# Kernel tuning notes

Measured on AMD Instinct MI355X. Metric: run time of the kernel, lower is better.

The kernel has to match this reference:

```python
import jax, jax.numpy as jnp
import numpy as np

SIG = [1, 1, 1, 1, -1]  # Cl(4,1)
NVEC = 5
GA = 1 << NVEC  # 32


def _build_gp_table():
    # Cayley table for the geometric product on blades indexed by bitmask.
    G = np.zeros((GA, GA, GA), np.float32)
    for a in range(GA):
        for b in range(GA):
            s = 0
            t = a >> 1
            while t:
                s += bin(t & b).count('1')
                t >>= 1
            sign = -1.0 if (s & 1) else 1.0
            common = a & b
            for i in range(NVEC):
                if (common >> i) & 1:
                    sign *= SIG[i]
            G[a, b, a ^ b] = sign
    return G

GP_TABLE = jnp.asarray(_build_gp_table())


def geometric_product(x, y):
    return jnp.einsum('...i,...j,ijk->...k', x, y, GP_TABLE)


def manifold_norm(x):
    # normalize each multivector onto the unit sphere in R^32
    return x / (jnp.linalg.norm(x, axis=-1, keepdims=True) + 1e-6)


def versor_linear(x, W, b):
    # channel mixing shared across multivector components: x [..., in, ga]
    return jnp.einsum('...ig,oi->...og', x, W) + b


def layer_norm2d(x, w, b):
    # LayerNorm over last two dims [D, ga] jointly
    mu = jnp.mean(x, axis=(-2, -1), keepdims=True)
    var = jnp.var(x, axis=(-2, -1), keepdims=True)
    return (x - mu) / jnp.sqrt(var + 1e-5) * w + b


def attention(x, Wq, bq, Wk, bk, Wv, bv, Wo, bo, n_heads):
    B, S, D, G = x.shape
    dh = D // n_heads
    q = versor_linear(x, Wq, bq).reshape(B, S, n_heads, dh, G)
    k = versor_linear(x, Wk, bk).reshape(B, S, n_heads, dh, G)
    v = versor_linear(x, Wv, bv).reshape(B, S, n_heads, dh, G)
    scale = 1.0 / np.sqrt(dh * G).astype(np.float32)
    scores = jnp.einsum('bshdg,bthdg->bhst', q, k) * scale
    probs = jax.nn.softmax(scores, axis=-1)
    o = jnp.einsum('bhst,bthdg->bshdg', probs, v).reshape(B, S, D, G)
    return versor_linear(o, Wo, bo)


N_HEADS = 8


def forward(x, Wq, bq, Wk, bk, Wv, bv, Wo, bo, ln1_w, ln1_b, ln2_w, ln2_b,
            gamma1, gamma2, W1, b1, W2, b2, Wr, br, Wc, bc):
    L = Wq.shape[0]
    for l in range(L):
        h = attention(layer_norm2d(x, ln1_w[l], ln1_b[l]),
                      Wq[l], bq[l], Wk[l], bk[l], Wv[l], bv[l], Wo[l], bo[l], N_HEADS)
        x = manifold_norm(x + gamma1[l] * h)
        m = versor_linear(layer_norm2d(x, ln2_w[l], ln2_b[l]), W1[l], b1[l])
        m = versor_linear(jnp.tanh(m), W2[l], b2[l])
        x = manifold_norm(x + gamma2[l] * m)
    # RecursiveRotorAccumulator: log(S)-step inclusive scan of rotors
    delta = versor_linear(x, Wr, br)
    rot = 0.5 * delta
    rot = rot.at[..., 0].add(1.0)
    rot = manifold_norm(rot)
    S = x.shape[1]
    step = 1
    while step < S:
        left = rot[:, :-step]
        right = rot[:, step:]
        comb = manifold_norm(geometric_product(right, left))
        rot = jnp.concatenate([rot[:, :step], comb], axis=1)
        step *= 2
    pooled = rot[:, -1]  # [B, D, ga]
    logits = pooled.reshape(pooled.shape[0], -1) @ Wc.T + bc
    return logits


def setup_inputs() -> dict:
    key = jax.random.key(0)
    B, S, D, G, L, NC = 8, 256, 64, GA, 4, 1000
    E = 4 * D  # expansion hidden
    ks = jax.random.split(key, 16)
    sd = 0.02
    inp = {
        'x': jax.random.normal(ks[0], (B, S, D, G), jnp.float32),
        'Wq': jax.random.normal(ks[1], (L, D, D), jnp.float32) * sd,
        'bq': jnp.zeros((L, D, G), jnp.float32),
        'Wk': jax.random.normal(ks[2], (L, D, D), jnp.float32) * sd,
        'bk': jnp.zeros((L, D, G), jnp.float32),
        'Wv': jax.random.normal(ks[3], (L, D, D), jnp.float32) * sd,
        'bv': jnp.zeros((L, D, G), jnp.float32),
        'Wo': jax.random.normal(ks[4], (L, D, D), jnp.float32) * sd,
        'bo': jnp.zeros((L, D, G), jnp.float32),
        'ln1_w': jnp.ones((L, D, G), jnp.float32),
        'ln1_b': jnp.zeros((L, D, G), jnp.float32),
        'ln2_w': jnp.ones((L, D, G), jnp.float32),
        'ln2_b': jnp.zeros((L, D, G), jnp.float32),
        'gamma1': 1e-5 * jnp.ones((L, D, G), jnp.float32),
        'gamma2': 1e-5 * jnp.ones((L, D, G), jnp.float32),
        'W1': jax.random.normal(ks[5], (L, E, D), jnp.float32) * sd,
        'b1': jnp.zeros((L, E, G), jnp.float32),
        'W2': jax.random.normal(ks[6], (L, D, E), jnp.float32) * sd,
        'b2': jnp.zeros((L, D, G), jnp.float32),
        'Wr': jax.random.normal(ks[7], (D, D), jnp.float32) * sd,
        'br': jnp.zeros((D, G), jnp.float32),
        'Wc': jax.random.normal(ks[8], (NC, D * G), jnp.float32) * sd,
        'bc': jnp.zeros((NC,), jnp.float32),
    }
    return inp


def reference(x, Wq, bq, Wk, bk, Wv, bv, Wo, bo, ln1_w, ln1_b, ln2_w, ln2_b,
              gamma1, gamma2, W1, b1, W2, b2, Wr, br, Wc, bc):
    return forward(x, Wq, bq, Wk, bk, Wv, bv, Wo, bo, ln1_w, ln1_b, ln2_w, ln2_b,
                   gamma1, gamma2, W1, b1, W2, b2, Wr, br, Wc, bc)
```

## Files before the change

kernel.cpp:

```cpp
#include <hip/hip_runtime.h>
#include <hip/hip_bf16.h>

constexpr int kB  = 8;
constexpr int kS  = 256;
constexpr int kD  = 64;
constexpr int kG  = 32;
constexpr int kE  = 256;
constexpr int kNH = 8;
constexpr int kHD = 256;
constexpr int kDG = kD * kG;
constexpr int kT  = kB * kS;
constexpr int kNC = 1000;

using bf16x8 = __attribute__((ext_vector_type(8))) short;
using f32x4  = __attribute__((ext_vector_type(4))) float;

__device__ __forceinline__ short f2bf(float f) {
    unsigned u = __float_as_uint(f);
    unsigned r = (u + 0x7FFFu + ((u >> 16) & 1u)) >> 16;
    return (short)r;
}

__device__ __forceinline__ float tanh_fast(float x) {
    float a = fabsf(x);
    float e = __expf(-2.f * a);
    float t = (1.f - e) / (1.f + e);
    return copysignf(t, x);
}

__global__ __launch_bounds__(256) void ln_kernel(const float* __restrict__ Xin,
                                                 const float* __restrict__ w,
                                                 const float* __restrict__ b,
                                                 float* __restrict__ A) {
    int t = blockIdx.x, tid = threadIdx.x;
    const float* xp = Xin + (size_t)t * kDG;
    __shared__ float r1[256], r2[256];
    float v[8], s = 0.f, ss = 0.f;
#pragma unroll
    for (int j = 0; j < 8; j++) {
        float x = xp[tid + j * 256];
        v[j] = x; s += x; ss += x * x;
    }
    r1[tid] = s; r2[tid] = ss; __syncthreads();
    for (int o = 128; o > 0; o >>= 1) {
        if (tid < o) { r1[tid] += r1[tid + o]; r2[tid] += r2[tid + o]; }
        __syncthreads();
    }
    float mean = r1[0] * (1.f / kDG);
    float var  = r2[0] * (1.f / kDG) - mean * mean;
    float rstd = rsqrtf(var + 1e-5f);
    float* ao = A + (size_t)t * kDG;
#pragma unroll
    for (int j = 0; j < 8; j++) {
        int jj = tid + j * 256;
        ao[jj] = (v[j] - mean) * rstd * w[jj] + b[jj];
    }
}

__device__ __forceinline__ void epi_res_mn_ln(
    const f32x4 (&acc)[4][2], const float* __restrict__ bias,
    const float* __restrict__ Xin, float* __restrict__ Xout,
    const float* __restrict__ gamma,
    const float* __restrict__ lnw, const float* __restrict__ lnb,
    float* __restrict__ Aout, int tok, int l16, int quad, bool do_ln) {
    const size_t tb = (size_t)tok * kDG;
    float xv[4][2][4];
    float s = 0.f, ss = 0.f;
#pragma unroll
    for (int mt = 0; mt < 4; ++mt)
#pragma unroll
        for (int r = 0; r < 4; ++r) {
            int o = mt * 16 + quad * 4 + r;
            float vv[2]; float sq = 0.f;
#pragma unroll
            for (int nt = 0; nt < 2; ++nt) {
                int g = nt * 16 + l16;
                float h = acc[mt][nt][r] + bias[o * kG + g];
                float v = Xin[tb + o * kG + g] + gamma[o * kG + g] * h;
                vv[nt] = v; sq = fmaf(v, v, sq);
            }
#pragma unroll
            for (int off = 1; off < 16; off <<= 1) sq += __shfl_xor(sq, off, 64);
            float rn = 1.f / (sqrtf(sq) + 1e-6f);
#pragma unroll
            for (int nt = 0; nt < 2; ++nt) {
                int g = nt * 16 + l16;
                float x = vv[nt] * rn;
                xv[mt][nt][r] = x;
                Xout[tb + o * kG + g] = x;
                s += x; ss = fmaf(x, x, ss);
            }
        }
    if (!do_ln) return;
#pragma unroll
    for (int off = 1; off < 64; off <<= 1) {
        s += __shfl_xor(s, off, 64); ss += __shfl_xor(ss, off, 64);
    }
    float mean = s * (1.f / kDG);
    float var  = ss * (1.f / kDG) - mean * mean;
    float rstd = rsqrtf(var + 1e-5f);
#pragma unroll
    for (int mt = 0; mt < 4; ++mt)
#pragma unroll
        for (int nt = 0; nt < 2; ++nt) {
            int g = nt * 16 + l16;
#pragma unroll
            for (int r = 0; r < 4; ++r) {
                int o = mt * 16 + quad * 4 + r;
                Aout[tb + o * kG + g] = (xv[mt][nt][r] - mean) * rstd * lnw[o * kG + g] + lnb[o * kG + g];
            }
        }
}

__global__ __launch_bounds__(256) void vlinT_kernel(const float* __restrict__ X,
                                                    const float* __restrict__ W,
                                                    const float* __restrict__ bias,
                                                    float* __restrict__ OutT) {
    __shared__ float sx[kDG];
    __shared__ float sw[kD * kD];
    int t = blockIdx.x, tid = threadIdx.x;
    const float* xp = X + (size_t)t * kDG;
    for (int j = tid; j < kDG; j += 256) sx[j] = xp[j];
    for (int j = tid; j < kD * kD; j += 256) sw[j] = W[j];
    __syncthreads();
    int g = tid & 31, ob = tid >> 5;
    int b = t >> 8, s = t & 255;
    float* op = OutT + ((size_t)b * kD * kS + s) * kG;
    for (int o = ob; o < kD; o += 8) {
        float acc = bias[o * kG + g];
        const float* wr = sw + o * kD;
#pragma unroll
        for (int i = 0; i < kD; i++) acc += wr[i] * sx[i * kG + g];
        op[(size_t)o * kS * kG + g] = acc;
    }
}

__global__ __launch_bounds__(256, 2) void mlp1_kernel(
    const float* __restrict__ X, const float* __restrict__ W,
    const float* __restrict__ bias, unsigned short* __restrict__ outH) {
    constexpr int M = 256;
    constexpr int WS = 64 + 8;
    __shared__ short sW[M * WS];
    __shared__ short sXT[4][32][WS];

    const int tid = threadIdx.x, wave = tid >> 6, lane = tid & 63;
    const int l16 = lane & 15, quad = lane >> 4;
    const int tok = blockIdx.x * 4 + wave;

    for (int j = tid * 4; j < M * 64; j += 1024) {
        const float4 w4 = *(const float4*)(W + j);
        int o = j >> 6, i = j & 63;
        *(short4*)&sW[o * WS + i] = make_short4(f2bf(w4.x), f2bf(w4.y), f2bf(w4.z), f2bf(w4.w));
    }
    {
        const int g4 = (lane & 7) * 4;
        const int i0 = (lane >> 3) * 8;
        const float* xp = X + (size_t)tok * kDG;
#pragma unroll
        for (int half = 0; half < 2; ++half) {
            float4 vr[4];
#pragma unroll
            for (int r = 0; r < 4; ++r)
                vr[r] = *(const float4*)(xp + (i0 + half * 4 + r) * kG + g4);
#pragma unroll
            for (int gg = 0; gg < 4; ++gg)
                *(short4*)&sXT[wave][g4 + gg][i0 + half * 4] =
                    make_short4(f2bf((&vr[0].x)[gg]), f2bf((&vr[1].x)[gg]),
                                f2bf((&vr[2].x)[gg]), f2bf((&vr[3].x)[gg]));
        }
    }
    __syncthreads();

    bf16x8 bfr[2][2];
#pragma unroll
    for (int c = 0; c < 2; ++c)
#pragma unroll
        for (int nt = 0; nt < 2; ++nt)
            bfr[c][nt] = *(const bf16x8*)&sXT[wave][nt * 16 + l16][c * 32 + quad * 8];

    f32x4 acc[16][2];
#pragma unroll
    for (int mt = 0; mt < 16; ++mt)
#pragma unroll
        for (int nt = 0; nt < 2; ++nt) acc[mt][nt] = (f32x4){0.f, 0.f, 0.f, 0.f};

#pragma unroll
    for (int mt = 0; mt < 16; ++mt)
#pragma unroll
        for (int c = 0; c < 2; ++c) {
            bf16x8 afr = *(const bf16x8*)&sW[(mt * 16 + l16) * WS + c * 32 + quad * 8];
#pragma unroll
            for (int nt = 0; nt < 2; ++nt)
                acc[mt][nt] = __builtin_amdgcn_mfma_f32_16x16x32_bf16(afr, bfr[c][nt], acc[mt][nt], 0, 0, 0);
        }

    unsigned short* op = outH + (size_t)tok * M * kG;
#pragma unroll
    for (int mt = 0; mt < 16; ++mt)
#pragma unroll
        for (int nt = 0; nt < 2; ++nt) {
            int g = nt * 16 + l16;
            int e0 = mt * 16 + quad * 4;
            short4 s4;
            s4.x = f2bf(tanh_fast(acc[mt][nt][0] + bias[(e0 + 0) * kG + g]));
            s4.y = f2bf(tanh_fast(acc[mt][nt][1] + bias[(e0 + 1) * kG + g]));
            s4.z = f2bf(tanh_fast(acc[mt][nt][2] + bias[(e0 + 2) * kG + g]));
            s4.w = f2bf(tanh_fast(acc[mt][nt][3] + bias[(e0 + 3) * kG + g]));
            *(short4*)&op[g * M + e0] = s4;
        }
}

__global__ __launch_bounds__(256, 2) void gemmWo_fused_kernel(
    const float* __restrict__ X, const float* __restrict__ W,
    const float* __restrict__ bias,
    const float* __restrict__ Xin, const float* __restrict__ gamma,
    const float* __restrict__ lnw, const float* __restrict__ lnb,
    float* __restrict__ Xout, float* __restrict__ Aout) {
    constexpr int WS = 64 + 8;
    __shared__ short sW[64 * WS];
    __shared__ short sXT[4][32][WS];

    const int tid = threadIdx.x, wave = tid >> 6, lane = tid & 63;
    const int l16 = lane & 15, quad = lane >> 4;
    const int tok = blockIdx.x * 4 + wave;

    for (int j = tid * 4; j < 64 * 64; j += 1024) {
        const float4 w4 = *(const float4*)(W + j);
        int o = j >> 6, i = j & 63;
        *(short4*)&sW[o * WS + i] = make_short4(f2bf(w4.x), f2bf(w4.y), f2bf(w4.z), f2bf(w4.w));
    }
    {
        const int g4 = (lane & 7) * 4;
        const int i0 = (lane >> 3) * 8;
        const float* xp = X + (size_t)tok * kDG;
#pragma unroll
        for (int half = 0; half < 2; ++half) {
            float4 vr[4];
#pragma unroll
            for (int r = 0; r < 4; ++r)
                vr[r] = *(const float4*)(xp + (i0 + half * 4 + r) * kG + g4);
#pragma unroll
            for (int gg = 0; gg < 4; ++gg)
                *(short4*)&sXT[wave][g4 + gg][i0 + half * 4] =
                    make_short4(f2bf((&vr[0].x)[gg]), f2bf((&vr[1].x)[gg]),
                                f2bf((&vr[2].x)[gg]), f2bf((&vr[3].x)[gg]));
        }
    }
    __syncthreads();

    bf16x8 bfr[2][2];
#pragma unroll
    for (int c = 0; c < 2; ++c)
#pragma unroll
        for (int nt = 0; nt < 2; ++nt)
            bfr[c][nt] = *(const bf16x8*)&sXT[wave][nt * 16 + l16][c * 32 + quad * 8];

    f32x4 acc[4][2];
#pragma unroll
    for (int mt = 0; mt < 4; ++mt)
#pragma unroll
        for (int nt = 0; nt < 2; ++nt) acc[mt][nt] = (f32x4){0.f, 0.f, 0.f, 0.f};

#pragma unroll
    for (int mt = 0; mt < 4; ++mt)
#pragma unroll
        for (int c = 0; c < 2; ++c) {
            bf16x8 afr = *(const bf16x8*)&sW[(mt * 16 + l16) * WS + c * 32 + quad * 8];
#pragma unroll
            for (int nt = 0; nt < 2; ++nt)
                acc[mt][nt] = __builtin_amdgcn_mfma_f32_16x16x32_bf16(afr, bfr[c][nt], acc[mt][nt], 0, 0, 0);
        }

    epi_res_mn_ln(acc, bias, Xin, Xout, gamma, lnw, lnb, Aout, tok, l16, quad, true);
}

__global__ __launch_bounds__(256, 2) void gemm_qkv_kernel(
    const float* __restrict__ X,
    const float* __restrict__ Wq, const float* __restrict__ Wk, const float* __restrict__ Wv,
    const float* __restrict__ bq, const float* __restrict__ bk, const float* __restrict__ bv,
    unsigned short* __restrict__ Q, unsigned short* __restrict__ K, unsigned short* __restrict__ V) {
    constexpr int WS = 64 + 8;
    __shared__ short sW[3 * 64 * WS];
    __shared__ short sXT[4][32][WS];

    const int tid = threadIdx.x, wave = tid >> 6, lane = tid & 63;
    const int l16 = lane & 15, quad = lane >> 4;
    const int tok = blockIdx.x * 4 + wave;

    const float* Wp[3] = {Wq, Wk, Wv};
#pragma unroll
    for (int w = 0; w < 3; ++w)
        for (int j = tid * 4; j < 64 * 64; j += 1024) {
            const float4 w4 = *(const float4*)(Wp[w] + j);
            int o = j >> 6, i = j & 63;
            *(short4*)&sW[w * 64 * WS + o * WS + i] =
                make_short4(f2bf(w4.x), f2bf(w4.y), f2bf(w4.z), f2bf(w4.w));
        }
    {
        const int g4 = (lane & 7) * 4;
        const int i0 = (lane >> 3) * 8;
        const float* xp = X + (size_t)tok * kDG;
#pragma unroll
        for (int half = 0; half < 2; ++half) {
            float4 vr[4];
#pragma unroll
            for (int r = 0; r < 4; ++r)
                vr[r] = *(const float4*)(xp + (i0 + half * 4 + r) * kG + g4);
#pragma unroll
            for (int gg = 0; gg < 4; ++gg)
                *(short4*)&sXT[wave][g4 + gg][i0 + half * 4] =
                    make_short4(f2bf((&vr[0].x)[gg]), f2bf((&vr[1].x)[gg]),
                                f2bf((&vr[2].x)[gg]), f2bf((&vr[3].x)[gg]));
        }
    }
    __syncthreads();

    bf16x8 bfr[2][2];
#pragma unroll
    for (int c = 0; c < 2; ++c)
#pragma unroll
        for (int nt = 0; nt < 2; ++nt)
            bfr[c][nt] = *(const bf16x8*)&sXT[wave][nt * 16 + l16][c * 32 + quad * 8];

    f32x4 acc[3][4][2];
#pragma unroll
    for (int w = 0; w < 3; ++w)
#pragma unroll
        for (int mt = 0; mt < 4; ++mt)
#pragma unroll
            for (int nt = 0; nt < 2; ++nt) acc[w][mt][nt] = (f32x4){0.f, 0.f, 0.f, 0.f};

#pragma unroll
    for (int w = 0; w < 3; ++w)
#pragma unroll
        for (int mt = 0; mt < 4; ++mt)
#pragma unroll
            for (int c = 0; c < 2; ++c) {
                bf16x8 afr = *(const bf16x8*)&sW[w * 64 * WS + (mt * 16 + l16) * WS + c * 32 + quad * 8];
#pragma unroll
                for (int nt = 0; nt < 2; ++nt)
                    acc[w][mt][nt] = __builtin_amdgcn_mfma_f32_16x16x32_bf16(afr, bfr[c][nt], acc[w][mt][nt], 0, 0, 0);
            }

    unsigned short* Op[3] = {Q, K, V};
    const float* Bp[3] = {bq, bk, bv};
#pragma unroll
    for (int w = 0; w < 3; ++w) {
        unsigned short* op = Op[w] + (size_t)tok * kDG;
#pragma unroll
        for (int mt = 0; mt < 4; ++mt)
#pragma unroll
            for (int nt = 0; nt < 2; ++nt) {
                int g = nt * 16 + l16;
#pragma unroll
                for (int r = 0; r < 4; ++r) {
                    int o = mt * 16 + quad * 4 + r;
                    op[o * kG + g] = (unsigned short)f2bf(acc[w][mt][nt][r] + Bp[w][o * kG + g]);
                }
            }
    }
}

template<bool DO_LN>
__global__ __launch_bounds__(256, 2) void mlp2_fused_kernel(
    const unsigned short* __restrict__ Mb,
    const float* __restrict__ W2, const float* __restrict__ b2,
    float* __restrict__ X, const float* __restrict__ gamma,
    const float* __restrict__ lnw, const float* __restrict__ lnb,
    float* __restrict__ Aout) {
    constexpr int WS = 256 + 8;
    __shared__ short sW[64 * WS];
    const int tid = threadIdx.x, wave = tid >> 6, lane = tid & 63;
    const int l16 = lane & 15, quad = lane >> 4;
    const int tok = blockIdx.x * 4 + wave;

    for (int j = tid * 4; j < 64 * 256; j += 1024) {
        const float4 w4 = *(const float4*)(W2 + j);
        int o = j >> 8, i = j & 255;
        *(short4*)&sW[o * WS + i] = make_short4(f2bf(w4.x), f2bf(w4.y), f2bf(w4.z), f2bf(w4.w));
    }
    __syncthreads();

    f32x4 acc[4][2];
#pragma unroll
    for (int mt = 0; mt < 4; ++mt)
#pragma unroll
        for (int nt = 0; nt < 2; ++nt) acc[mt][nt] = (f32x4){0.f, 0.f, 0.f, 0.f};

    const unsigned short* mp = Mb + (size_t)tok * kG * kE;
#pragma unroll
    for (int c = 0; c < 8; ++c) {
        bf16x8 bfr[2];
#pragma unroll
        for (int nt = 0; nt < 2; ++nt)
            bfr[nt] = *(const bf16x8*)&mp[(nt * 16 + l16) * kE + c * 32 + quad * 8];
#pragma unroll
        for (int mt = 0; mt < 4; ++mt) {
            bf16x8 afr = *(const bf16x8*)&sW[(mt * 16 + l16) * WS + c * 32 + quad * 8];
#pragma unroll
            for (int nt = 0; nt < 2; ++nt)
                acc[mt][nt] = __builtin_amdgcn_mfma_f32_16x16x32_bf16(afr, bfr[nt], acc[mt][nt], 0, 0, 0);
        }
    }

    epi_res_mn_ln(acc, b2, X, X, gamma, lnw, lnb, Aout, tok, l16, quad, DO_LN);
}

constexpr int QSTR = 264;
constexpr int VSTR = 40;

__global__ __launch_bounds__(256) void attn_mfma_kernel(const unsigned short* __restrict__ Q,
                                                        const unsigned short* __restrict__ K,
                                                        const unsigned short* __restrict__ V,
                                                        float* __restrict__ O) {
    __shared__ short sQ[64 * QSTR];
    __shared__ short sKV[256 * VSTR];

    const int qt = blockIdx.x, h = blockIdx.y, b = blockIdx.z;
    const int tid = threadIdx.x;
    const int wave = tid >> 6, lane = tid & 63;
    const int l16 = lane & 15, quad = lane >> 4;

    const size_t bh = (size_t)b * kS * kDG + (size_t)h * kHD;

#pragma unroll
    for (int it = 0; it < 8; ++it) {
        int j = it * 2048 + tid * 8;
        int row = j >> 8, col = j & 255;
        *(bf16x8*)&sQ[row * QSTR + col] =
            *(const bf16x8*)(Q + bh + (size_t)(qt * 64 + row) * kDG + col);
    }
    __syncthreads();

    bf16x8 afrag[8];
    {
        int row = wave * 16 + l16;
#pragma unroll
        for (int c = 0; c < 8; ++c)
            afrag[c] = *(const bf16x8*)&sQ[row * QSTR + c * 32 + quad * 8];
    }

    f32x4 acc[16];
#pragma unroll
    for (int i = 0; i < 16; ++i) acc[i] = (f32x4){0.f, 0.f, 0.f, 0.f};

    for (int kt = 0; kt < 8; ++kt) {
        __syncthreads();
#pragma unroll
        for (int it = 0; it < 4; ++it) {
            int j = it * 2048 + tid * 8;
            int row = j >> 8, col = j & 255;
            *(bf16x8*)&sKV[row * QSTR + col] =
                *(const bf16x8*)(K + bh + (size_t)(kt * 32 + row) * kDG + col);
        }
        __syncthreads();
#pragma unroll
        for (int nt = 0; nt < 2; ++nt) {
            int key = nt * 16 + l16;
            f32x4 a = acc[kt * 2 + nt];
#pragma unroll
            for (int c = 0; c < 8; ++c) {
                bf16x8 bfrag = *(const bf16x8*)&sKV[key * QSTR + c * 32 + quad * 8];
                a = __builtin_amdgcn_mfma_f32_16x16x32_bf16(afrag[c], bfrag, a, 0, 0, 0);
            }
            acc[kt * 2 + nt] = a;
        }
    }
    __syncthreads();

    float inv[4];
#pragma unroll
    for (int r = 0; r < 4; ++r) {
        float m = -1e30f;
#pragma unroll
        for (int t = 0; t < 16; ++t) m = fmaxf(m, acc[t][r]);
#pragma unroll
        for (int off = 1; off < 16; off <<= 1) m = fmaxf(m, __shfl_xor(m, off, 16));
        float s = 0.f;
#pragma unroll
        for (int t = 0; t < 16; ++t) {
            float p = __expf((acc[t][r] - m) * 0.0625f);
            acc[t][r] = p; s += p;
        }
#pragma unroll
        for (int off = 1; off < 16; off <<= 1) s += __shfl_xor(s, off, 16);
        inv[r] = 1.f / s;
    }

#pragma unroll
    for (int t = 0; t < 16; ++t)
#pragma unroll
        for (int r = 0; r < 4; ++r)
            sQ[(wave * 16 + quad * 4 + r) * QSTR + t * 16 + l16] = f2bf(acc[t][r]);

    f32x4 oacc[16];
#pragma unroll
    for (int i = 0; i < 16; ++i) oacc[i] = (f32x4){0.f, 0.f, 0.f, 0.f};

    for (int vt = 0; vt < 8; ++vt) {
        __syncthreads();
        {
            int kb = tid >> 5;
#pragma unroll
            for (int it = 0; it < 2; ++it) {
                int db = (tid & 31) + it * 32;
                short4 vr[4];
#pragma unroll
                for (int r = 0; r < 4; ++r)
                    vr[r] = *(const short4*)(V + bh + (size_t)(vt * 32 + kb * 4 + r) * kDG + db * 4);
#pragma unroll
                for (int i = 0; i < 4; ++i) {
                    short4 p = make_short4((&vr[0].x)[i], (&vr[1].x)[i],
                                           (&vr[2].x)[i], (&vr[3].x)[i]);
                    *(short4*)&sKV[(db * 4 + i) * VSTR + kb * 4] = p;
                }
            }
        }
        __syncthreads();
        bf16x8 pfrag = *(const bf16x8*)&sQ[(wave * 16 + l16) * QSTR + vt * 32 + quad * 8];
#pragma unroll
        for (int dt = 0; dt < 16; ++dt) {
            bf16x8 vfrag = *(const bf16x8*)&sKV[(dt * 16 + l16) * VSTR + quad * 8];
            oacc[dt] = __builtin_amdgcn_mfma_f32_16x16x32_bf16(pfrag, vfrag, oacc[dt], 0, 0, 0);
        }
    }

    {
        int qrow = qt * 64 + wave * 16 + quad * 4;
#pragma unroll
        for (int dt = 0; dt < 16; ++dt)
#pragma unroll
            for (int r = 0; r < 4; ++r)
                O[bh + (size_t)(qrow + r) * kDG + dt * 16 + l16] = oacc[dt][r] * inv[r];
    }
}

constexpr int pc_ce(unsigned v) { int c = 0; while (v) { c += v & 1; v >>= 1; } return c; }
constexpr unsigned gp_mask_ce(int a) {
    unsigned m = 0;
    for (int c = 0; c < 32; ++c) {
        int b = a ^ c;
        int s = (a & b) >> 4;
        for (int t = a >> 1; t; t >>= 1) s += pc_ce(t & b);
        if (s & 1) m |= (1u << c);
    }
    return m;
}

template<int A>
__device__ __forceinline__ void gp_term(const float* x, const float* y, float* acc) {
    constexpr unsigned m = gp_mask_ce(A);
    const float xa = x[A], nxa = -xa;
#pragma unroll
    for (int c = 0; c < 32; ++c)
        acc[c] = fmaf(((m >> c) & 1u) ? nxa : xa, y[A ^ c], acc[c]);
}

__device__ __forceinline__ void gp_mn_t(const float* x, const float* y, float* out) {
    float acc[32];
#pragma unroll
    for (int c = 0; c < 32; ++c) acc[c] = 0.f;
    gp_term<0>(x, y, acc);  gp_term<1>(x, y, acc);  gp_term<2>(x, y, acc);  gp_term<3>(x, y, acc);
    gp_term<4>(x, y, acc);  gp_term<5>(x, y, acc);  gp_term<6>(x, y, acc);  gp_term<7>(x, y, acc);
    gp_term<8>(x, y, acc);  gp_term<9>(x, y, acc);  gp_term<10>(x, y, acc); gp_term<11>(x, y, acc);
    gp_term<12>(x, y, acc); gp_term<13>(x, y, acc); gp_term<14>(x, y, acc); gp_term<15>(x, y, acc);
    gp_term<16>(x, y, acc); gp_term<17>(x, y, acc); gp_term<18>(x, y, acc); gp_term<19>(x, y, acc);
    gp_term<20>(x, y, acc); gp_term<21>(x, y, acc); gp_term<22>(x, y, acc); gp_term<23>(x, y, acc);
    gp_term<24>(x, y, acc); gp_term<25>(x, y, acc); gp_term<26>(x, y, acc); gp_term<27>(x, y, acc);
    gp_term<28>(x, y, acc); gp_term<29>(x, y, acc); gp_term<30>(x, y, acc); gp_term<31>(x, y, acc);
    float ss = 0.f;
#pragma unroll
    for (int c = 0; c < 32; ++c) ss = fmaf(acc[c], acc[c], ss);
    float r = 1.f / (sqrtf(ss) + 1e-6f);
#pragma unroll
    for (int c = 0; c < 32; ++c) out[c] = acc[c] * r;
}

__device__ __forceinline__ void leaf_load(const float* base, float* v) {
#pragma unroll
    for (int i = 0; i < 8; ++i) {
        const float4 f = *(const float4*)(base + i * 4);
        v[i * 4 + 0] = 0.5f * f.x; v[i * 4 + 1] = 0.5f * f.y;
        v[i * 4 + 2] = 0.5f * f.z; v[i * 4 + 3] = 0.5f * f.w;
    }
    v[0] += 1.f;
    float ss = 0.f;
#pragma unroll
    for (int c = 0; c < 32; ++c) ss = fmaf(v[c], v[c], ss);
    float r = 1.f / (sqrtf(ss) + 1e-6f);
#pragma unroll
    for (int c = 0; c < 32; ++c) v[c] *= r;
}

__global__ __launch_bounds__(256) void scanreg_kernel(const float* __restrict__ DT,
                                                      float* __restrict__ pooled) {
    const int wave = threadIdx.x >> 6, lane = threadIdx.x & 63;
    const int seq = blockIdx.x * 4 + wave;
    const float* base = DT + ((size_t)seq * kS + lane * 4) * kG;

    float R[32], Y[32], P[32], Xa[32], Yb[32];

    leaf_load(base, R);
    for (int j = 1; j < 4; ++j) {
        leaf_load(base + j * kG, Y);
        gp_mn_t(Y, R, R);
    }

    for (int step = 1; step < 64; step <<= 1) {
        const bool up = lane & step;
#pragma unroll
        for (int c = 0; c < 32; ++c) P[c] = __shfl_xor(R[c], step, 64);
#pragma unroll
        for (int c = 0; c < 32; ++c) {
            Xa[c] = up ? R[c] : P[c];
            Yb[c] = up ? P[c] : R[c];
        }
        gp_mn_t(Xa, Yb, R);
    }

    if (lane == 0) {
        float* op = pooled + (size_t)seq * kG;
#pragma unroll
        for (int i = 0; i < 8; ++i)
            *(float4*)(op + i * 4) = make_float4(R[i * 4], R[i * 4 + 1], R[i * 4 + 2], R[i * 4 + 3]);
    }
}

__global__ __launch_bounds__(256) void cls2_kernel(const float* __restrict__ P,
                                                   const float* __restrict__ Wc,
                                                   const float* __restrict__ bc,
                                                   float* __restrict__ out) {
    __shared__ float sp[kB * kDG];
    const int tid = threadIdx.x, wave = tid >> 6, lane = tid & 63;
    for (int j = tid * 4; j < kB * kDG; j += 1024)
        *(float4*)&sp[j] = *(const float4*)(P + j);
    __syncthreads();

    const int c = blockIdx.x * 4 + wave;
    const float* w = Wc + (size_t)c * kDG;
    float acc[kB];
#pragma unroll
    for (int b = 0; b < kB; ++b) acc[b] = 0.f;
#pragma unroll
    for (int cc = 0; cc < 8; ++cc) {
        const float4 w4 = *(const float4*)(w + cc * 256 + lane * 4);
#pragma unroll
        for (int b = 0; b < kB; ++b) {
            const float4 p4 = *(const float4*)&sp[b * kDG + cc * 256 + lane * 4];
            acc[b] += w4.x * p4.x + w4.y * p4.y + w4.z * p4.z + w4.w * p4.w;
        }
    }
#pragma unroll
    for (int b = 0; b < kB; ++b)
#pragma unroll
        for (int off = 32; off > 0; off >>= 1) acc[b] += __shfl_xor(acc[b], off, 64);
    if (lane == 0) {
        float bias = bc[c];
#pragma unroll
        for (int b = 0; b < kB; ++b) out[b * kNC + c] = acc[b] + bias;
    }
}

extern "C" void kernel_launch(void* const* d_in, const int* in_sizes, int n_in,
                              void* d_out, int out_size, void* d_ws, size_t ws_size,
                              hipStream_t stream) {
    const float* x_in = (const float*)d_in[0];
    const float* Wq   = (const float*)d_in[1];
    const float* bq   = (const float*)d_in[2];
    const float* Wk   = (const float*)d_in[3];
    const float* bk   = (const float*)d_in[4];
    const float* Wv   = (const float*)d_in[5];
    const float* bv   = (const float*)d_in[6];
    const float* Wo   = (const float*)d_in[7];
    const float* bo   = (const float*)d_in[8];
    const float* ln1w = (const float*)d_in[9];
    const float* ln1b = (const float*)d_in[10];
    const float* ln2w = (const float*)d_in[11];
    const float* ln2b = (const float*)d_in[12];
    const float* gm1  = (const float*)d_in[13];
    const float* gm2  = (const float*)d_in[14];
    const float* W1   = (const float*)d_in[15];
    const float* b1   = (const float*)d_in[16];
    const float* W2   = (const float*)d_in[17];
    const float* b2   = (const float*)d_in[18];
    const float* Wr   = (const float*)d_in[19];
    const float* br   = (const float*)d_in[20];
    const float* Wc   = (const float*)d_in[21];
    const float* bc   = (const float*)d_in[22];

    const size_t NEL = (size_t)kT * kDG;
    float* F  = (float*)d_ws;
    float* X  = F;
    float* A  = F + NEL;
    float* Qb = F + 2 * NEL;
    float* Kb = F + 3 * NEL;
    float* Vb = F + 4 * NEL;
    unsigned short* Qh = (unsigned short*)Qb;
    unsigned short* Kh = (unsigned short*)Kb;
    unsigned short* Vh = (unsigned short*)Vb;
    unsigned short* Mb = (unsigned short*)Kb;
    float* pooled = Qb;

    ln_kernel<<<kT, 256, 0, stream>>>(x_in, ln1w, ln1b, A);

    for (int l = 0; l < 4; l++) {
        gemm_qkv_kernel<<<kT / 4, 256, 0, stream>>>(A,
            Wq + l * kD * kD, Wk + l * kD * kD, Wv + l * kD * kD,
            bq + l * kDG, bk + l * kDG, bv + l * kDG, Qh, Kh, Vh);
        attn_mfma_kernel<<<dim3(4, kNH, kB), 256, 0, stream>>>(Qh, Kh, Vh, A);
        gemmWo_fused_kernel<<<kT / 4, 256, 0, stream>>>(A, Wo + l * kD * kD, bo + l * kDG,
            l == 0 ? x_in : X, gm1 + l * kDG, ln2w + l * kDG, ln2b + l * kDG, X, A);
        mlp1_kernel<<<kT / 4, 256, 0, stream>>>(A, W1 + l * kE * kD, b1 + l * kE * kG, Mb);
        if (l < 3)
            mlp2_fused_kernel<true><<<kT / 4, 256, 0, stream>>>(Mb, W2 + l * kD * kE, b2 + l * kDG,
                X, gm2 + l * kDG, ln1w + (l + 1) * kDG, ln1b + (l + 1) * kDG, A);
        else
            mlp2_fused_kernel<false><<<kT / 4, 256, 0, stream>>>(Mb, W2 + l * kD * kE, b2 + l * kDG,
                X, gm2 + l * kDG, nullptr, nullptr, nullptr);
    }

    vlinT_kernel<<<kT, 256, 0, stream>>>(X, Wr, br, A);
    scanreg_kernel<<<kB * kD / 4, 256, 0, stream>>>(A, pooled);
    cls2_kernel<<<kNC / 4, 256, 0, stream>>>(pooled, Wc, bc, (float*)d_out);
}
```

Measured before the change: 610.6 us.

## Fuse Wo projection with MLP1 and MLP2 with next-layer QKV projection

Merges the attention output projection (with residual, manifold norm and LayerNorm) into the first MLP GEMM, keeping the normalized activations in shared memory as bf16 instead of writing the fp32 A buffer and re-reading it. Also fuses the second MLP GEMM epilogue with the next layer's QKV projection, so the post-LN activations never round-trip through global memory. This cuts five kernels per layer to three and removes several full-tensor fp32 reads and writes. The cost is larger shared-memory footprints and more register pressure per block, which may lower occupancy.

```diff
diff --git a/kernel.cpp b/kernel.cpp
--- a/kernel.cpp
+++ b/kernel.cpp
@@ -57,15 +57,570 @@
     }
 }
 
-__device__ __forceinline__ void epi_res_mn_ln(
-    const f32x4 (&acc)[4][2], const float* __restrict__ bias,
-    const float* __restrict__ Xin, float* __restrict__ Xout,
-    const float* __restrict__ gamma,
+__global__ __launch_bounds__(256, 2) void gemm_qkv0_kernel(
+    const float* __restrict__ X,
+    const float* __restrict__ Wq, const float* __restrict__ Wk, const float* __restrict__ Wv,
+    const float* __restrict__ bq, const float* __restrict__ bk, const float* __restrict__ bv,
+    unsigned short* __restrict__ Q, unsigned short* __restrict__ K, unsigned short* __restrict__ V) {
+    constexpr int WS = 64 + 8;
+    __shared__ short sW[3 * 64 * WS];
+    __shared__ short sXT[4][32][WS];
+
+    const int tid = threadIdx.x, wave = tid >> 6, lane = tid & 63;
+    const int l16 = lane & 15, quad = lane >> 4;
+    const int tok = blockIdx.x * 4 + wave;
+
+    const float* Wp[3] = {Wq, Wk, Wv};
+#pragma unroll
+    for (int w = 0; w < 3; ++w)
+        for (int j = tid * 4; j < 64 * 64; j += 1024) {
+            const float4 w4 = *(const float4*)(Wp[w] + j);
+            int o = j >> 6, i = j & 63;
+            *(short4*)&sW[w * 64 * WS + o * WS + i] =
+                make_short4(f2bf(w4.x), f2bf(w4.y), f2bf(w4.z), f2bf(w4.w));
+        }
+    {
+        const int g4 = (lane & 7) * 4;
+        const int i0 = (lane >> 3) * 8;
+        const float* xp = X + (size_t)tok * kDG;
+#pragma unroll
+        for (int half = 0; half < 2; ++half) {
+            float4 vr[4];
+#pragma unroll
+            for (int r = 0; r < 4; ++r)
+                vr[r] = *(const float4*)(xp + (i0 + half * 4 + r) * kG + g4);
+#pragma unroll
+            for (int gg = 0; gg < 4; ++gg)
+                *(short4*)&sXT[wave][g4 + gg][i0 + half * 4] =
+                    make_short4(f2bf((&vr[0].x)[gg]), f2bf((&vr[1].x)[gg]),
+                                f2bf((&vr[2].x)[gg]), f2bf((&vr[3].x)[gg]));
+        }
+    }
+    __syncthreads();
+
+    bf16x8 bfr[2][2];
+#pragma unroll
+    for (int c = 0; c < 2; ++c)
+#pragma unroll
+        for (int nt = 0; nt < 2; ++nt)
+            bfr[c][nt] = *(const bf16x8*)&sXT[wave][nt * 16 + l16][c * 32 + quad * 8];
+
+    f32x4 acc[3][4][2];
+#pragma unroll
+    for (int w = 0; w < 3; ++w)
+#pragma unroll
+        for (int mt = 0; mt < 4; ++mt)
+#pragma unroll
+            for (int nt = 0; nt < 2; ++nt) acc[w][mt][nt] = (f32x4){0.f, 0.f, 0.f, 0.f};
+
+#pragma unroll
+    for (int w = 0; w < 3; ++w)
+#pragma unroll
+        for (int mt = 0; mt < 4; ++mt)
+#pragma unroll
+            for (int c = 0; c < 2; ++c) {
+                bf16x8 afr = *(const bf16x8*)&sW[w * 64 * WS + (mt * 16 + l16) * WS + c * 32 + quad * 8];
+#pragma unroll
+                for (int nt = 0; nt < 2; ++nt)
+                    acc[w][mt][nt] = __builtin_amdgcn_mfma_f32_16x16x32_bf16(afr, bfr[c][nt], acc[w][mt][nt], 0, 0, 0);
+            }
+
+    unsigned short* Op[3] = {Q, K, V};
+    const float* Bp[3] = {bq, bk, bv};
+#pragma unroll
+    for (int w = 0; w < 3; ++w) {
+        unsigned short* op = Op[w] + (size_t)tok * kDG;
+#pragma unroll
+        for (int mt = 0; mt < 4; ++mt)
+#pragma unroll
+            for (int nt = 0; nt < 2; ++nt) {
+                int g = nt * 16 + l16;
+#pragma unroll
+                for (int r = 0; r < 4; ++r) {
+                    int o = mt * 16 + quad * 4 + r;
+                    op[o * kG + g] = (unsigned short)f2bf(acc[w][mt][nt][r] + Bp[w][o * kG + g]);
+                }
+            }
+    }
+}
+
+constexpr int QSTR = 264;
+constexpr int VSTR = 40;
+
+__global__ __launch_bounds__(256) void attn_mfma_kernel(const unsigned short* __restrict__ Q,
+                                                        const unsigned short* __restrict__ K,
+                                                        const unsigned short* __restrict__ V,
+                                                        float* __restrict__ O) {
+    __shared__ short sQ[64 * QSTR];
+    __shared__ short sKV[256 * VSTR];
+
+    const int qt = blockIdx.x, h = blockIdx.y, b = blockIdx.z;
+    const int tid = threadIdx.x;
+    const int wave = tid >> 6, lane = tid & 63;
+    const int l16 = lane & 15, quad = lane >> 4;
+
+    const size_t bh = (size_t)b * kS * kDG + (size_t)h * kHD;
+
+#pragma unroll
+    for (int it = 0; it < 8; ++it) {
+        int j = it * 2048 + tid * 8;
+        int row = j >> 8, col = j & 255;
+        *(bf16x8*)&sQ[row * QSTR + col] =
+            *(const bf16x8*)(Q + bh + (size_t)(qt * 64 + row) * kDG + col);
+    }
+    __syncthreads();
+
+    bf16x8 afrag[8];
+    {
+        int row = wave * 16 + l16;
+#pragma unroll
+        for (int c = 0; c < 8; ++c)
+            afrag[c] = *(const bf16x8*)&sQ[row * QSTR + c * 32 + quad * 8];
+    }
+
+    f32x4 acc[16];
+#pragma unroll
+    for (int i = 0; i < 16; ++i) acc[i] = (f32x4){0.f, 0.f, 0.f, 0.f};
+
+    for (int kt = 0; kt < 8; ++kt) {
+        __syncthreads();
+#pragma unroll
+        for (int it = 0; it < 4; ++it) {
+            int j = it * 2048 + tid * 8;
+            int row = j >> 8, col = j & 255;
+            *(bf16x8*)&sKV[row * QSTR + col] =
+                *(const bf16x8*)(K + bh + (size_t)(kt * 32 + row) * kDG + col);
+        }
+        __syncthreads();
+#pragma unroll
+        for (int nt = 0; nt < 2; ++nt) {
+            int key = nt * 16 + l16;
+            f32x4 a = acc[kt * 2 + nt];
+#pragma unroll
+            for (int c = 0; c < 8; ++c) {
+                bf16x8 bfrag = *(const bf16x8*)&sKV[key * QSTR + c * 32 + quad * 8];
+                a = __builtin_amdgcn_mfma_f32_16x16x32_bf16(afrag[c], bfrag, a, 0, 0, 0);
+            }
+            acc[kt * 2 + nt] = a;
+        }
+    }
+    __syncthreads();
+
+    float inv[4];
+#pragma unroll
+    for (int r = 0; r < 4; ++r) {
+        float m = -1e30f;
+#pragma unroll
+        for (int t = 0; t < 16; ++t) m = fmaxf(m, acc[t][r]);
+#pragma unroll
+        for (int off = 1; off < 16; off <<= 1) m = fmaxf(m, __shfl_xor(m, off, 16));
+        float s = 0.f;
+#pragma unroll
+        for (int t = 0; t < 16; ++t) {
+            float p = __expf((acc[t][r] - m) * 0.0625f);
+            acc[t][r] = p; s += p;
+        }
+#pragma unroll
+        for (int off = 1; off < 16; off <<= 1) s += __shfl_xor(s, off, 16);
+        inv[r] = 1.f / s;
+    }
+
+#pragma unroll
+    for (int t = 0; t < 16; ++t)
+#pragma unroll
+        for (int r = 0; r < 4; ++r)
+            sQ[(wave * 16 + quad * 4 + r) * QSTR + t * 16 + l16] = f2bf(acc[t][r]);
+
+    f32x4 oacc[16];
+#pragma unroll
+    for (int i = 0; i < 16; ++i) oacc[i] = (f32x4){0.f, 0.f, 0.f, 0.f};
+
+    for (int vt = 0; vt < 8; ++vt) {
+        __syncthreads();
+        {
+            int kb = tid >> 5;
+#pragma unroll
+            for (int it = 0; it < 2; ++it) {
+                int db = (tid & 31) + it * 32;
+                short4 vr[4];
+#pragma unroll
+                for (int r = 0; r < 4; ++r)
+                    vr[r] = *(const short4*)(V + bh + (size_t)(vt * 32 + kb * 4 + r) * kDG + db * 4);
+#pragma unroll
+                for (int i = 0; i < 4; ++i) {
+                    short4 p = make_short4((&vr[0].x)[i], (&vr[1].x)[i],
+                                           (&vr[2].x)[i], (&vr[3].x)[i]);
+                    *(short4*)&sKV[(db * 4 + i) * VSTR + kb * 4] = p;
+                }
+            }
+        }
+        __syncthreads();
+        bf16x8 pfrag = *(const bf16x8*)&sQ[(wave * 16 + l16) * QSTR + vt * 32 + quad * 8];
+#pragma unroll
+        for (int dt = 0; dt < 16; ++dt) {
+            bf16x8 vfrag = *(const bf16x8*)&sKV[(dt * 16 + l16) * VSTR + quad * 8];
+            oacc[dt] = __builtin_amdgcn_mfma_f32_16x16x32_bf16(pfrag, vfrag, oacc[dt], 0, 0, 0);
+        }
+    }
+
+    {
+        int qrow = qt * 64 + wave * 16 + quad * 4;
+#pragma unroll
+        for (int dt = 0; dt < 16; ++dt)
+#pragma unroll
+            for (int r = 0; r < 4; ++r)
+                O[bh + (size_t)(qrow + r) * kDG + dt * 16 + l16] = oacc[dt][r] * inv[r];
+    }
+}
+
+__global__ __launch_bounds__(256, 2) void womlp1_kernel(
+    const float* __restrict__ O,
+    const float* __restrict__ Wo, const float* __restrict__ bo,
+    const float* __restrict__ Xin, const float* __restrict__ gamma,
     const float* __restrict__ lnw, const float* __restrict__ lnb,
-    float* __restrict__ Aout, int tok, int l16, int quad, bool do_ln) {
+    const float* __restrict__ W1, const float* __restrict__ b1,
+    float* __restrict__ Xout, unsigned short* __restrict__ Mb) {
+    constexpr int WS = 64 + 8;
+    __shared__ short sWo[64 * WS];
+    __shared__ short sW1[256 * WS];
+    __shared__ short sXT[4][32][WS];
+
+    const int tid = threadIdx.x, wave = tid >> 6, lane = tid & 63;
+    const int l16 = lane & 15, quad = lane >> 4;
+    const int tok = blockIdx.x * 4 + wave;
+
+    for (int j = tid * 4; j < 64 * 64; j += 1024) {
+        const float4 w4 = *(const float4*)(Wo + j);
+        int o = j >> 6, i = j & 63;
+        *(short4*)&sWo[o * WS + i] = make_short4(f2bf(w4.x), f2bf(w4.y), f2bf(w4.z), f2bf(w4.w));
+    }
+    for (int j = tid * 4; j < 256 * 64; j += 1024) {
+        const float4 w4 = *(const float4*)(W1 + j);
+        int o = j >> 6, i = j & 63;
+        *(short4*)&sW1[o * WS + i] = make_short4(f2bf(w4.x), f2bf(w4.y), f2bf(w4.z), f2bf(w4.w));
+    }
+    {
+        const int g4 = (lane & 7) * 4;
+        const int i0 = (lane >> 3) * 8;
+        const float* xp = O + (size_t)tok * kDG;
+#pragma unroll
+        for (int half = 0; half < 2; ++half) {
+            float4 vr[4];
+#pragma unroll
+            for (int r = 0; r < 4; ++r)
+                vr[r] = *(const float4*)(xp + (i0 + half * 4 + r) * kG + g4);
+#pragma unroll
+            for (int gg = 0; gg < 4; ++gg)
+                *(short4*)&sXT[wave][g4 + gg][i0 + half * 4] =
+                    make_short4(f2bf((&vr[0].x)[gg]), f2bf((&vr[1].x)[gg]),
+                                f2bf((&vr[2].x)[gg]), f2bf((&vr[3].x)[gg]));
+        }
+    }
+    __syncthreads();
+
+    bf16x8 bfr[2][2];
+#pragma unroll
+    for (int c = 0; c < 2; ++c)
+#pragma unroll
+        for (int nt = 0; nt < 2; ++nt)
+            bfr[c][nt] = *(const bf16x8*)&sXT[wave][nt * 16 + l16][c * 32 + quad * 8];
+
+    f32x4 acc[4][2];
+#pragma unroll
+    for (int mt = 0; mt < 4; ++mt)
+#pragma unroll
+        for (int nt = 0; nt < 2; ++nt) acc[mt][nt] = (f32x4){0.f, 0.f, 0.f, 0.f};
+#pragma unroll
+    for (int mt = 0; mt < 4; ++mt)
+#pragma unroll
+        for (int c = 0; c < 2; ++c) {
+            bf16x8 afr = *(const bf16x8*)&sWo[(mt * 16 + l16) * WS + c * 32 + quad * 8];
+#pragma unroll
+            for (int nt = 0; nt < 2; ++nt)
+                acc[mt][nt] = __builtin_amdgcn_mfma_f32_16x16x32_bf16(afr, bfr[c][nt], acc[mt][nt], 0, 0, 0);
+        }
+
+    {
+        const size_t tb = (size_t)tok * kDG;
+        float xv[4][2][4];
+        float s = 0.f, ss = 0.f;
+#pragma unroll
+        for (int mt = 0; mt < 4; ++mt)
+#pragma unroll
+            for (int r = 0; r < 4; ++r) {
+                int o = mt * 16 + quad * 4 + r;
+                float vv[2]; float sq = 0.f;
+#pragma unroll
+                for (int nt = 0; nt < 2; ++nt) {
+                    int g = nt * 16 + l16;
+                    float h = acc[mt][nt][r] + bo[o * kG + g];
+                    float v = Xin[tb + o * kG + g] + gamma[o * kG + g] * h;
+                    vv[nt] = v; sq = fmaf(v, v, sq);
+                }
+#pragma unroll
+                for (int off = 1; off < 16; off <<= 1) sq += __shfl_xor(sq, off, 64);
+                float rn = 1.f / (sqrtf(sq) + 1e-6f);
+#pragma unroll
+                for (int nt = 0; nt < 2; ++nt) {
+                    int g = nt * 16 + l16;
+                    float x = vv[nt] * rn;
+                    xv[mt][nt][r] = x;
+                    Xout[tb + o * kG + g] = x;
+                    s += x; ss = fmaf(x, x, ss);
+                }
+            }
+#pragma unroll
+        for (int off = 1; off < 64; off <<= 1) {
+            s += __shfl_xor(s, off, 64); ss += __shfl_xor(ss, off, 64);
+        }
+        float mean = s * (1.f / kDG);
+        float var  = ss * (1.f / kDG) - mean * mean;
+        float rstd = rsqrtf(var + 1e-5f);
+#pragma unroll
+        for (int mt = 0; mt < 4; ++mt)
+#pragma unroll
+            for (int nt = 0; nt < 2; ++nt) {
+                int g = nt * 16 + l16;
+                short4 s4;
+#pragma unroll
+                for (int r = 0; r < 4; ++r) {
+                    int o = mt * 16 + quad * 4 + r;
+                    ((short*)&s4)[r] = f2bf((xv[mt][nt][r] - mean) * rstd * lnw[o * kG + g] + lnb[o * kG + g]);
+                }
+                *(short4*)&sXT[wave][g][mt * 16 + quad * 4] = s4;
+            }
+    }
+
+    bf16x8 b2fr[2][2];
+#pragma unroll
+    for (int c = 0; c < 2; ++c)
+#pragma unroll
+        for (int nt = 0; nt < 2; ++nt)
+            b2fr[c][nt] = *(const bf16x8*)&sXT[wave][nt * 16 + l16][c * 32 + quad * 8];
+
+    f32x4 acc2[16][2];
+#pragma unroll
+    for (int mt = 0; mt < 16; ++mt)
+#pragma unroll
+        for (int nt = 0; nt < 2; ++nt) acc2[mt][nt] = (f32x4){0.f, 0.f, 0.f, 0.f};
+#pragma unroll
+    for (int mt = 0; mt < 16; ++mt)
+#pragma unroll
+        for (int c = 0; c < 2; ++c) {
+            bf16x8 afr = *(const bf16x8*)&sW1[(mt * 16 + l16) * WS + c * 32 + quad * 8];
+#pragma unroll
+            for (int nt = 0; nt < 2; ++nt)
+                acc2[mt][nt] = __builtin_amdgcn_mfma_f32_16x16x32_bf16(afr, b2fr[c][nt], acc2[mt][nt], 0, 0, 0);
+        }
+
+    unsigned short* op = Mb + (size_t)tok * kE * kG;
+#pragma unroll
+    for (int mt = 0; mt < 16; ++mt)
+#pragma unroll
+        for (int nt = 0; nt < 2; ++nt) {
+            int g = nt * 16 + l16;
+            int e0 = mt * 16 + quad * 4;
+            short4 s4;
+            s4.x = f2bf(tanh_fast(acc2[mt][nt][0] + b1[(e0 + 0) * kG + g]));
+            s4.y = f2bf(tanh_fast(acc2[mt][nt][1] + b1[(e0 + 1) * kG + g]));
+            s4.z = f2bf(tanh_fast(acc2[mt][nt][2] + b1[(e0 + 2) * kG + g]));
+            s4.w = f2bf(tanh_fast(acc2[mt][nt][3] + b1[(e0 + 3) * kG + g]));
+            *(short4*)&op[g * kE + e0] = s4;
+        }
+}
+
+__global__ __launch_bounds__(256, 2) void mlp2qkv_kernel(
+    const unsigned short* __restrict__ Mb,
+    const float* __restrict__ W2, const float* __restrict__ b2,
+    float* __restrict__ X, const float* __restrict__ gamma,
+    const float* __restrict__ lnw, const float* __restrict__ lnb,
+    const float* __restrict__ Wq, const float* __restrict__ Wk, const float* __restrict__ Wv,
+    const float* __restrict__ bq, const float* __restrict__ bk, const float* __restrict__ bv,
+    unsigned short* __restrict__ Q, unsigned short* __restrict__ K, unsigned short* __restrict__ V) {
+    constexpr int W2S = 256 + 8;
+    constexpr int WS  = 64 + 8;
+    __shared__ short sW2[64 * W2S];
+    __shared__ short sWqkv[3 * 64 * WS];
+    __shared__ short sA1[4][32][WS];
+
+    const int tid = threadIdx.x, wave = tid >> 6, lane = tid & 63;
+    const int l16 = lane & 15, quad = lane >> 4;
+    const int tok = blockIdx.x * 4 + wave;
+
+    for (int j = tid * 4; j < 64 * 256; j += 1024) {
+        const float4 w4 = *(const float4*)(W2 + j);
+        int o = j >> 8, i = j & 255;
+        *(short4*)&sW2[o * W2S + i] = make_short4(f2bf(w4.x), f2bf(w4.y), f2bf(w4.z), f2bf(w4.w));
+    }
+    const float* Wp[3] = {Wq, Wk, Wv};
+#pragma unroll
+    for (int w = 0; w < 3; ++w)
+        for (int j = tid * 4; j < 64 * 64; j += 1024) {
+            const float4 w4 = *(const float4*)(Wp[w] + j);
+            int o = j >> 6, i = j & 63;
+            *(short4*)&sWqkv[w * 64 * WS + o * WS + i] =
+                make_short4(f2bf(w4.x), f2bf(w4.y), f2bf(w4.z), f2bf(w4.w));
+        }
+    __syncthreads();
+
+    f32x4 acc[4][2];
+#pragma unroll
+    for (int mt = 0; mt < 4; ++mt)
+#pragma unroll
+        for (int nt = 0; nt < 2; ++nt) acc[mt][nt] = (f32x4){0.f, 0.f, 0.f, 0.f};
+
+    const unsigned short* mp = Mb + (size_t)tok * kG * kE;
+#pragma unroll
+    for (int c = 0; c < 8; ++c) {
+        bf16x8 bfr[2];
+#pragma unroll
+        for (int nt = 0; nt < 2; ++nt)
+            bfr[nt] = *(const bf16x8*)&mp[(nt * 16 + l16) * kE + c * 32 + quad * 8];
+#pragma unroll
+        for (int mt = 0; mt < 4; ++mt) {
+            bf16x8 afr = *(const bf16x8*)&sW2[(mt * 16 + l16) * W2S + c * 32 + quad * 8];
+#pragma unroll
+            for (int nt = 0; nt < 2; ++nt)
+                acc[mt][nt] = __builtin_amdgcn_mfma_f32_16x16x32_bf16(afr, bfr[nt], acc[mt][nt], 0, 0, 0);
+        }
+    }
+
+    {
+        const size_t tb = (size_t)tok * kDG;
+        float xv[4][2][4];
+        float s = 0.f, ss = 0.f;
+#pragma unroll
+        for (int mt = 0; mt < 4; ++mt)
+#pragma unroll
+            for (int r = 0; r < 4; ++r) {
+                int o = mt * 16 + quad * 4 + r;
+                float vv[2]; float sq = 0.f;
+#pragma unroll
+                for (int nt = 0; nt < 2; ++nt) {
+                    int g = nt * 16 + l16;
+                    float h = acc[mt][nt][r] + b2[o * kG + g];
+                    float v = X[tb + o * kG + g] + gamma[o * kG + g] * h;
+                    vv[nt] = v; sq = fmaf(v, v, sq);
+                }
+#pragma unroll
+                for (int off = 1; off < 16; off <<= 1) sq += __shfl_xor(sq, off, 64);
+                float rn = 1.f / (sqrtf(sq) + 1e-6f);
+#pragma unroll
+                for (int nt = 0; nt < 2; ++nt) {
+                    int g = nt * 16 + l16;
+                    float x = vv[nt] * rn;
+                    xv[mt][nt][r] = x;
+                    X[tb + o * kG + g] = x;
+                    s += x; ss = fmaf(x, x, ss);
+                }
+            }
+#pragma unroll
+        for (int off = 1; off < 64; off <<= 1) {
+            s += __shfl_xor(s, off, 64); ss += __shfl_xor(ss, off, 64);
+        }
+        float mean = s * (1.f / kDG);
+        float var  = ss * (1.f / kDG) - mean * mean;
+        float rstd = rsqrtf(var + 1e-5f);
+#pragma unroll
+        for (int mt = 0; mt < 4; ++mt)
+#pragma unroll
+            for (int nt = 0; nt < 2; ++nt) {
+                int g = nt * 16 + l16;
+                short4 s4;
+#pragma unroll
+                for (int r = 0; r < 4; ++r) {
+                    int o = mt * 16 + quad * 4 + r;
+                    ((short*)&s4)[r] = f2bf((xv[mt][nt][r] - mean) * rstd * lnw[o * kG + g] + lnb[o * kG + g]);
+                }
+                *(short4*)&sA1[wave][g][mt * 16 + quad * 4] = s4;
+            }
+    }
+
+    bf16x8 bq1[2][2];
+#pragma unroll
+    for (int c = 0; c < 2; ++c)
+#pragma unroll
+        for (int nt = 0; nt < 2; ++nt)
+            bq1[c][nt] = *(const bf16x8*)&sA1[wave][nt * 16 + l16][c * 32 + quad * 8];
+
+    f32x4 qacc[3][4][2];
+#pragma unroll
+    for (int w = 0; w < 3; ++w)
+#pragma unroll
+        for (int mt = 0; mt < 4; ++mt)
+#pragma unroll
+            for (int nt = 0; nt < 2; ++nt) qacc[w][mt][nt] = (f32x4){0.f, 0.f, 0.f, 0.f};
+#pragma unroll
+    for (int w = 0; w < 3; ++w)
+#pragma unroll
+        for (int mt = 0; mt < 4; ++mt)
+#pragma unroll
+            for (int c = 0; c < 2; ++c) {
+                bf16x8 afr = *(const bf16x8*)&sWqkv[w * 64 * WS + (mt * 16 + l16) * WS + c * 32 + quad * 8];
+#pragma unroll
+                for (int nt = 0; nt < 2; ++nt)
+                    qacc[w][mt][nt] = __builtin_amdgcn_mfma_f32_16x16x32_bf16(afr, bq1[c][nt], qacc[w][mt][nt], 0, 0, 0);
+            }
+
+    unsigned short* Op[3] = {Q, K, V};
+    const float* Bp[3] = {bq, bk, bv};
+#pragma unroll
+    for (int w = 0; w < 3; ++w) {
+        unsigned short* op = Op[w] + (size_t)tok * kDG;
+#pragma unroll
+        for (int mt = 0; mt < 4; ++mt)
+#pragma unroll
+            for (int nt = 0; nt < 2; ++nt) {
+                int g = nt * 16 + l16;
+#pragma unroll
+                for (int r = 0; r < 4; ++r) {
+                    int o = mt * 16 + quad * 4 + r;
+                    op[o * kG + g] = (unsigned short)f2bf(qacc[w][mt][nt][r] + Bp[w][o * kG + g]);
+                }
+            }
+    }
+}
+
+__global__ __launch_bounds__(256, 2) void mlp2_plain_kernel(
+    const unsigned short* __restrict__ Mb,
+    const float* __restrict__ W2, const float* __restrict__ b2,
+    float* __restrict__ X, const float* __restrict__ gamma) {
+    constexpr int W2S = 256 + 8;
+    __shared__ short sW2[64 * W2S];
+    const int tid = threadIdx.x, wave = tid >> 6, lane = tid & 63;
+    const int l16 = lane & 15, quad = lane >> 4;
+    const int tok = blockIdx.x * 4 + wave;
+
+    for (int j = tid * 4; j < 64 * 256; j += 1024) {
+        const float4 w4 = *(const float4*)(W2 + j);
+        int o = j >> 8, i = j & 255;
+        *(short4*)&sW2[o * W2S + i] = make_short4(f2bf(w4.x), f2bf(w4.y), f2bf(w4.z), f2bf(w4.w));
+    }
+    __syncthreads();
+
+    f32x4 acc[4][2];
+#pragma unroll
+    for (int mt = 0; mt < 4; ++mt)
+#pragma unroll
+        for (int nt = 0; nt < 2; ++nt) acc[mt][nt] = (f32x4){0.f, 0.f, 0.f, 0.f};
+
+    const unsigned short* mp = Mb + (size_t)tok * kG * kE;
+#pragma unroll
+    for (int c = 0; c < 8; ++c) {
+        bf16x8 bfr[2];
+#pragma unroll
+        for (int nt = 0; nt < 2; ++nt)
+            bfr[nt] = *(const bf16x8*)&mp[(nt * 16 + l16) * kE + c * 32 + quad * 8];
+#pragma unroll
+        for (int mt = 0; mt < 4; ++mt) {
+            bf16x8 afr = *(const bf16x8*)&sW2[(mt * 16 + l16) * W2S + c * 32 + quad * 8];
+#pragma unroll
+            for (int nt = 0; nt < 2; ++nt)
+                acc[mt][nt] = __builtin_amdgcn_mfma_f32_16x16x32_bf16(afr, bfr[nt], acc[mt][nt], 0, 0, 0);
+        }
+    }
+
     const size_t tb = (size_t)tok * kDG;
-    float xv[4][2][4];
-    float s = 0.f, ss = 0.f;
 #pragma unroll
     for (int mt = 0; mt < 4; ++mt)
 #pragma unroll
@@ -75,8 +630,8 @@
 #pragma unroll
             for (int nt = 0; nt < 2; ++nt) {
                 int g = nt * 16 + l16;
-                float h = acc[mt][nt][r] + bias[o * kG + g];
-                float v = Xin[tb + o * kG + g] + gamma[o * kG + g] * h;
+                float h = acc[mt][nt][r] + b2[o * kG + g];
+                float v = X[tb + o * kG + g] + gamma[o * kG + g] * h;
                 vv[nt] = v; sq = fmaf(v, v, sq);
             }
 #pragma unroll
@@ -85,29 +640,7 @@
 #pragma unroll
             for (int nt = 0; nt < 2; ++nt) {
                 int g = nt * 16 + l16;
-                float x = vv[nt] * rn;
-                xv[mt][nt][r] = x;
-                Xout[tb + o * kG + g] = x;
-                s += x; ss = fmaf(x, x, ss);
-            }
-        }
-    if (!do_ln) return;
-#pragma unroll
-    for (int off = 1; off < 64; off <<= 1) {
-        s += __shfl_xor(s, off, 64); ss += __shfl_xor(ss, off, 64);
-    }
-    float mean = s * (1.f / kDG);
-    float var  = ss * (1.f / kDG) - mean * mean;
-    float rstd = rsqrtf(var + 1e-5f);
-#pragma unroll
-    for (int mt = 0; mt < 4; ++mt)
-#pragma unroll
-        for (int nt = 0; nt < 2; ++nt) {
-            int g = nt * 16 + l16;
-#pragma unroll
-            for (int r = 0; r < 4; ++r) {
-                int o = mt * 16 + quad * 4 + r;
-                Aout[tb + o * kG + g] = (xv[mt][nt][r] - mean) * rstd * lnw[o * kG + g] + lnb[o * kG + g];
+                X[tb + o * kG + g] = vv[nt] * rn;
             }
         }
 }
@@ -132,406 +665,6 @@
 #pragma unroll
         for (int i = 0; i < kD; i++) acc += wr[i] * sx[i * kG + g];
         op[(size_t)o * kS * kG + g] = acc;
-    }
-}
-
-__global__ __launch_bounds__(256, 2) void mlp1_kernel(
-    const float* __restrict__ X, const float* __restrict__ W,
-    const float* __restrict__ bias, unsigned short* __restrict__ outH) {
-    constexpr int M = 256;
-    constexpr int WS = 64 + 8;
-    __shared__ short sW[M * WS];
-    __shared__ short sXT[4][32][WS];
-
-    const int tid = threadIdx.x, wave = tid >> 6, lane = tid & 63;
-    const int l16 = lane & 15, quad = lane >> 4;
-    const int tok = blockIdx.x * 4 + wave;
-
-    for (int j = tid * 4; j < M * 64; j += 1024) {
-        const float4 w4 = *(const float4*)(W + j);
-        int o = j >> 6, i = j & 63;
-        *(short4*)&sW[o * WS + i] = make_short4(f2bf(w4.x), f2bf(w4.y), f2bf(w4.z), f2bf(w4.w));
-    }
-    {
-        const int g4 = (lane & 7) * 4;
-        const int i0 = (lane >> 3) * 8;
-        const float* xp = X + (size_t)tok * kDG;
-#pragma unroll
-        for (int half = 0; half < 2; ++half) {
-            float4 vr[4];
-#pragma unroll
-            for (int r = 0; r < 4; ++r)
-                vr[r] = *(const float4*)(xp + (i0 + half * 4 + r) * kG + g4);
-#pragma unroll
-            for (int gg = 0; gg < 4; ++gg)
-                *(short4*)&sXT[wave][g4 + gg][i0 + half * 4] =
-                    make_short4(f2bf((&vr[0].x)[gg]), f2bf((&vr[1].x)[gg]),
-                                f2bf((&vr[2].x)[gg]), f2bf((&vr[3].x)[gg]));
-        }
-    }
-    __syncthreads();
-
-    bf16x8 bfr[2][2];
-#pragma unroll
-    for (int c = 0; c < 2; ++c)
-#pragma unroll
-        for (int nt = 0; nt < 2; ++nt)
-            bfr[c][nt] = *(const bf16x8*)&sXT[wave][nt * 16 + l16][c * 32 + quad * 8];
-
-    f32x4 acc[16][2];
-#pragma unroll
-    for (int mt = 0; mt < 16; ++mt)
-#pragma unroll
-        for (int nt = 0; nt < 2; ++nt) acc[mt][nt] = (f32x4){0.f, 0.f, 0.f, 0.f};
-
-#pragma unroll
-    for (int mt = 0; mt < 16; ++mt)
-#pragma unroll
-        for (int c = 0; c < 2; ++c) {
-            bf16x8 afr = *(const bf16x8*)&sW[(mt * 16 + l16) * WS + c * 32 + quad * 8];
-#pragma unroll
-            for (int nt = 0; nt < 2; ++nt)
-                acc[mt][nt] = __builtin_amdgcn_mfma_f32_16x16x32_bf16(afr, bfr[c][nt], acc[mt][nt], 0, 0, 0);
-        }
-
-    unsigned short* op = outH + (size_t)tok * M * kG;
-#pragma unroll
-    for (int mt = 0; mt < 16; ++mt)
-#pragma unroll
-        for (int nt = 0; nt < 2; ++nt) {
-            int g = nt * 16 + l16;
-            int e0 = mt * 16 + quad * 4;
-            short4 s4;
-            s4.x = f2bf(tanh_fast(acc[mt][nt][0] + bias[(e0 + 0) * kG + g]));
-            s4.y = f2bf(tanh_fast(acc[mt][nt][1] + bias[(e0 + 1) * kG + g]));
-            s4.z = f2bf(tanh_fast(acc[mt][nt][2] + bias[(e0 + 2) * kG + g]));
-            s4.w = f2bf(tanh_fast(acc[mt][nt][3] + bias[(e0 + 3) * kG + g]));
-            *(short4*)&op[g * M + e0] = s4;
-        }
-}
-
-__global__ __launch_bounds__(256, 2) void gemmWo_fused_kernel(
-    const float* __restrict__ X, const float* __restrict__ W,
-    const float* __restrict__ bias,
-    const float* __restrict__ Xin, const float* __restrict__ gamma,
-    const float* __restrict__ lnw, const float* __restrict__ lnb,
-    float* __restrict__ Xout, float* __restrict__ Aout) {
-    constexpr int WS = 64 + 8;
-    __shared__ short sW[64 * WS];
-    __shared__ short sXT[4][32][WS];
-
-    const int tid = threadIdx.x, wave = tid >> 6, lane = tid & 63;
-    const int l16 = lane & 15, quad = lane >> 4;
-    const int tok = blockIdx.x * 4 + wave;
-
-    for (int j = tid * 4; j < 64 * 64; j += 1024) {
-        const float4 w4 = *(const float4*)(W + j);
-        int o = j >> 6, i = j & 63;
-        *(short4*)&sW[o * WS + i] = make_short4(f2bf(w4.x), f2bf(w4.y), f2bf(w4.z), f2bf(w4.w));
-    }
-    {
-        const int g4 = (lane & 7) * 4;
-        const int i0 = (lane >> 3) * 8;
-        const float* xp = X + (size_t)tok * kDG;
-#pragma unroll
-        for (int half = 0; half < 2; ++half) {
-            float4 vr[4];
-#pragma unroll
-            for (int r = 0; r < 4; ++r)
-                vr[r] = *(const float4*)(xp + (i0 + half * 4 + r) * kG + g4);
-#pragma unroll
-            for (int gg = 0; gg < 4; ++gg)
-                *(short4*)&sXT[wave][g4 + gg][i0 + half * 4] =
-                    make_short4(f2bf((&vr[0].x)[gg]), f2bf((&vr[1].x)[gg]),
-                                f2bf((&vr[2].x)[gg]), f2bf((&vr[3].x)[gg]));
-        }
-    }
-    __syncthreads();
-
-    bf16x8 bfr[2][2];
-#pragma unroll
-    for (int c = 0; c < 2; ++c)
-#pragma unroll
-        for (int nt = 0; nt < 2; ++nt)
-            bfr[c][nt] = *(const bf16x8*)&sXT[wave][nt * 16 + l16][c * 32 + quad * 8];
-
-    f32x4 acc[4][2];
-#pragma unroll
-    for (int mt = 0; mt < 4; ++mt)
-#pragma unroll
-        for (int nt = 0; nt < 2; ++nt) acc[mt][nt] = (f32x4){0.f, 0.f, 0.f, 0.f};
-
-#pragma unroll
-    for (int mt = 0; mt < 4; ++mt)
-#pragma unroll
-        for (int c = 0; c < 2; ++c) {
-            bf16x8 afr = *(const bf16x8*)&sW[(mt * 16 + l16) * WS + c * 32 + quad * 8];
-#pragma unroll
-            for (int nt = 0; nt < 2; ++nt)
-                acc[mt][nt] = __builtin_amdgcn_mfma_f32_16x16x32_bf16(afr, bfr[c][nt], acc[mt][nt], 0, 0, 0);
-        }
-
-    epi_res_mn_ln(acc, bias, Xin, Xout, gamma, lnw, lnb, Aout, tok, l16, quad, true);
-}
-
-__global__ __launch_bounds__(256, 2) void gemm_qkv_kernel(
-    const float* __restrict__ X,
-    const float* __restrict__ Wq, const float* __restrict__ Wk, const float* __restrict__ Wv,
-    const float* __restrict__ bq, const float* __restrict__ bk, const float* __restrict__ bv,
-    unsigned short* __restrict__ Q, unsigned short* __restrict__ K, unsigned short* __restrict__ V) {
-    constexpr int WS = 64 + 8;
-    __shared__ short sW[3 * 64 * WS];
-    __shared__ short sXT[4][32][WS];
-
-    const int tid = threadIdx.x, wave = tid >> 6, lane = tid & 63;
-    const int l16 = lane & 15, quad = lane >> 4;
-    const int tok = blockIdx.x * 4 + wave;
-
-    const float* Wp[3] = {Wq, Wk, Wv};
-#pragma unroll
-    for (int w = 0; w < 3; ++w)
-        for (int j = tid * 4; j < 64 * 64; j += 1024) {
-            const float4 w4 = *(const float4*)(Wp[w] + j);
-            int o = j >> 6, i = j & 63;
-            *(short4*)&sW[w * 64 * WS + o * WS + i] =
-                make_short4(f2bf(w4.x), f2bf(w4.y), f2bf(w4.z), f2bf(w4.w));
-        }
-    {
-        const int g4 = (lane & 7) * 4;
-        const int i0 = (lane >> 3) * 8;
-        const float* xp = X + (size_t)tok * kDG;
-#pragma unroll
-        for (int half = 0; half < 2; ++half) {
-            float4 vr[4];
-#pragma unroll
-            for (int r = 0; r < 4; ++r)
-                vr[r] = *(const float4*)(xp + (i0 + half * 4 + r) * kG + g4);
-#pragma unroll
-            for (int gg = 0; gg < 4; ++gg)
-                *(short4*)&sXT[wave][g4 + gg][i0 + half * 4] =
-                    make_short4(f2bf((&vr[0].x)[gg]), f2bf((&vr[1].x)[gg]),
-                                f2bf((&vr[2].x)[gg]), f2bf((&vr[3].x)[gg]));
-        }
-    }
-    __syncthreads();
-
-    bf16x8 bfr[2][2];
-#pragma unroll
-    for (int c = 0; c < 2; ++c)
-#pragma unroll
-        for (int nt = 0; nt < 2; ++nt)
-            bfr[c][nt] = *(const bf16x8*)&sXT[wave][nt * 16 + l16][c * 32 + quad * 8];
-
-    f32x4 acc[3][4][2];
-#pragma unroll
-    for (int w = 0; w < 3; ++w)
-#pragma unroll
-        for (int mt = 0; mt < 4; ++mt)
-#pragma unroll
-            for (int nt = 0; nt < 2; ++nt) acc[w][mt][nt] = (f32x4){0.f, 0.f, 0.f, 0.f};
-
-#pragma unroll
-    for (int w = 0; w < 3; ++w)
-#pragma unroll
-        for (int mt = 0; mt < 4; ++mt)
-#pragma unroll
-            for (int c = 0; c < 2; ++c) {
-                bf16x8 afr = *(const bf16x8*)&sW[w * 64 * WS + (mt * 16 + l16) * WS + c * 32 + quad * 8];
-#pragma unroll
-                for (int nt = 0; nt < 2; ++nt)
-                    acc[w][mt][nt] = __builtin_amdgcn_mfma_f32_16x16x32_bf16(afr, bfr[c][nt], acc[w][mt][nt], 0, 0, 0);
-            }
-
-    unsigned short* Op[3] = {Q, K, V};
-    const float* Bp[3] = {bq, bk, bv};
-#pragma unroll
-    for (int w = 0; w < 3; ++w) {
-        unsigned short* op = Op[w] + (size_t)tok * kDG;
-#pragma unroll
-        for (int mt = 0; mt < 4; ++mt)
-#pragma unroll
-            for (int nt = 0; nt < 2; ++nt) {
-                int g = nt * 16 + l16;
-#pragma unroll
-                for (int r = 0; r < 4; ++r) {
-                    int o = mt * 16 + quad * 4 + r;
-                    op[o * kG + g] = (unsigned short)f2bf(acc[w][mt][nt][r] + Bp[w][o * kG + g]);
-                }
-            }
-    }
-}
-
-template<bool DO_LN>
-__global__ __launch_bounds__(256, 2) void mlp2_fused_kernel(
-    const unsigned short* __restrict__ Mb,
-    const float* __restrict__ W2, const float* __restrict__ b2,
-    float* __restrict__ X, const float* __restrict__ gamma,
-    const float* __restrict__ lnw, const float* __restrict__ lnb,
-    float* __restrict__ Aout) {
-    constexpr int WS = 256 + 8;
-    __shared__ short sW[64 * WS];
-    const int tid = threadIdx.x, wave = tid >> 6, lane = tid & 63;
-    const int l16 = lane & 15, quad = lane >> 4;
-    const int tok = blockIdx.x * 4 + wave;
-
-    for (int j = tid * 4; j < 64 * 256; j += 1024) {
-        const float4 w4 = *(const float4*)(W2 + j);
-        int o = j >> 8, i = j & 255;
-        *(short4*)&sW[o * WS + i] = make_short4(f2bf(w4.x), f2bf(w4.y), f2bf(w4.z), f2bf(w4.w));
-    }
-    __syncthreads();
-
-    f32x4 acc[4][2];
-#pragma unroll
-    for (int mt = 0; mt < 4; ++mt)
-#pragma unroll
-        for (int nt = 0; nt < 2; ++nt) acc[mt][nt] = (f32x4){0.f, 0.f, 0.f, 0.f};
-
-    const unsigned short* mp = Mb + (size_t)tok * kG * kE;
-#pragma unroll
-    for (int c = 0; c < 8; ++c) {
-        bf16x8 bfr[2];
-#pragma unroll
-        for (int nt = 0; nt < 2; ++nt)
-            bfr[nt] = *(const bf16x8*)&mp[(nt * 16 + l16) * kE + c * 32 + quad * 8];
-#pragma unroll
-        for (int mt = 0; mt < 4; ++mt) {
-            bf16x8 afr = *(const bf16x8*)&sW[(mt * 16 + l16) * WS + c * 32 + quad * 8];
-#pragma unroll
-            for (int nt = 0; nt < 2; ++nt)
-                acc[mt][nt] = __builtin_amdgcn_mfma_f32_16x16x32_bf16(afr, bfr[nt], acc[mt][nt], 0, 0, 0);
-        }
-    }
-
-    epi_res_mn_ln(acc, b2, X, X, gamma, lnw, lnb, Aout, tok, l16, quad, DO_LN);
-}
-
-constexpr int QSTR = 264;
-constexpr int VSTR = 40;
-
-__global__ __launch_bounds__(256) void attn_mfma_kernel(const unsigned short* __restrict__ Q,
-                                                        const unsigned short* __restrict__ K,
-                                                        const unsigned short* __restrict__ V,
-                                                        float* __restrict__ O) {
-    __shared__ short sQ[64 * QSTR];
-    __shared__ short sKV[256 * VSTR];
-
-    const int qt = blockIdx.x, h = blockIdx.y, b = blockIdx.z;
-    const int tid = threadIdx.x;
-    const int wave = tid >> 6, lane = tid & 63;
-    const int l16 = lane & 15, quad = lane >> 4;
-
-    const size_t bh = (size_t)b * kS * kDG + (size_t)h * kHD;
-
-#pragma unroll
-    for (int it = 0; it < 8; ++it) {
-        int j = it * 2048 + tid * 8;
-        int row = j >> 8, col = j & 255;
-        *(bf16x8*)&sQ[row * QSTR + col] =
-            *(const bf16x8*)(Q + bh + (size_t)(qt * 64 + row) * kDG + col);
-    }
-    __syncthreads();
-
-    bf16x8 afrag[8];
-    {
-        int row = wave * 16 + l16;
-#pragma unroll
-        for (int c = 0; c < 8; ++c)
-            afrag[c] = *(const bf16x8*)&sQ[row * QSTR + c * 32 + quad * 8];
-    }
-
-    f32x4 acc[16];
-#pragma unroll
-    for (int i = 0; i < 16; ++i) acc[i] = (f32x4){0.f, 0.f, 0.f, 0.f};
-
-    for (int kt = 0; kt < 8; ++kt) {
-        __syncthreads();
-#pragma unroll
-        for (int it = 0; it < 4; ++it) {
-            int j = it * 2048 + tid * 8;
-            int row = j >> 8, col = j & 255;
-            *(bf16x8*)&sKV[row * QSTR + col] =
-                *(const bf16x8*)(K + bh + (size_t)(kt * 32 + row) * kDG + col);
-        }
-        __syncthreads();
-#pragma unroll
-        for (int nt = 0; nt < 2; ++nt) {
-            int key = nt * 16 + l16;
-            f32x4 a = acc[kt * 2 + nt];
-#pragma unroll
-            for (int c = 0; c < 8; ++c) {
-                bf16x8 bfrag = *(const bf16x8*)&sKV[key * QSTR + c * 32 + quad * 8];
-                a = __builtin_amdgcn_mfma_f32_16x16x32_bf16(afrag[c], bfrag, a, 0, 0, 0);
-            }
-            acc[kt * 2 + nt] = a;
-        }
-    }
-    __syncthreads();
-
-    float inv[4];
-#pragma unroll
-    for (int r = 0; r < 4; ++r) {
-        float m = -1e30f;
-#pragma unroll
-        for (int t = 0; t < 16; ++t) m = fmaxf(m, acc[t][r]);
-#pragma unroll
-        for (int off = 1; off < 16; off <<= 1) m = fmaxf(m, __shfl_xor(m, off, 16));
-        float s = 0.f;
-#pragma unroll
-        for (int t = 0; t < 16; ++t) {
-            float p = __expf((acc[t][r] - m) * 0.0625f);
-            acc[t][r] = p; s += p;
-        }
-#pragma unroll
-        for (int off = 1; off < 16; off <<= 1) s += __shfl_xor(s, off, 16);
-        inv[r] = 1.f / s;
-    }
-
-#pragma unroll
-    for (int t = 0; t < 16; ++t)
-#pragma unroll
-        for (int r = 0; r < 4; ++r)
-            sQ[(wave * 16 + quad * 4 + r) * QSTR + t * 16 + l16] = f2bf(acc[t][r]);
-
-    f32x4 oacc[16];
-#pragma unroll
-    for (int i = 0; i < 16; ++i) oacc[i] = (f32x4){0.f, 0.f, 0.f, 0.f};
-
-    for (int vt = 0; vt < 8; ++vt) {
-        __syncthreads();
-        {
-            int kb = tid >> 5;
-#pragma unroll
-            for (int it = 0; it < 2; ++it) {
-                int db = (tid & 31) + it * 32;
-                short4 vr[4];
-#pragma unroll
-                for (int r = 0; r < 4; ++r)
-                    vr[r] = *(const short4*)(V + bh + (size_t)(vt * 32 + kb * 4 + r) * kDG + db * 4);
-#pragma unroll
-                for (int i = 0; i < 4; ++i) {
-                    short4 p = make_short4((&vr[0].x)[i], (&vr[1].x)[i],
-                                           (&vr[2].x)[i], (&vr[3].x)[i]);
-                    *(short4*)&sKV[(db * 4 + i) * VSTR + kb * 4] = p;
-                }
-            }
-        }
-        __syncthreads();
-        bf16x8 pfrag = *(const bf16x8*)&sQ[(wave * 16 + l16) * QSTR + vt * 32 + quad * 8];
-#pragma unroll
-        for (int dt = 0; dt < 16; ++dt) {
-            bf16x8 vfrag = *(const bf16x8*)&sKV[(dt * 16 + l16) * VSTR + quad * 8];
-            oacc[dt] = __builtin_amdgcn_mfma_f32_16x16x32_bf16(pfrag, vfrag, oacc[dt], 0, 0, 0);
-        }
-    }
-
-    {
-        int qrow = qt * 64 + wave * 16 + quad * 4;
-#pragma unroll
-        for (int dt = 0; dt < 16; ++dt)
-#pragma unroll
-            for (int r = 0; r < 4; ++r)
-                O[bh + (size_t)(qrow + r) * kDG + dt * 16 + l16] = oacc[dt][r] * inv[r];
     }
 }
 
@@ -691,35 +824,33 @@
     const size_t NEL = (size_t)kT * kDG;
     float* F  = (float*)d_ws;
     float* X  = F;
-    float* A  = F + NEL;
-    float* Qb = F + 2 * NEL;
-    float* Kb = F + 3 * NEL;
-    float* Vb = F + 4 * NEL;
-    unsigned short* Qh = (unsigned short*)Qb;
-    unsigned short* Kh = (unsigned short*)Kb;
-    unsigned short* Vh = (unsigned short*)Vb;
-    unsigned short* Mb = (unsigned short*)Kb;
-    float* pooled = Qb;
-
-    ln_kernel<<<kT, 256, 0, stream>>>(x_in, ln1w, ln1b, A);
+    float* Ob = F + NEL;
+    unsigned short* Qh = (unsigned short*)(F + 2 * NEL);
+    unsigned short* Kh = (unsigned short*)(F + 3 * NEL);
+    unsigned short* Vh = (unsigned short*)(F + 4 * NEL);
+    unsigned short* Mb = (unsigned short*)(F + 5 * NEL);
+    float* DT = Ob;
+    float* pooled = F + 2 * NEL;
+
+    ln_kernel<<<kT, 256, 0, stream>>>(x_in, ln1w, ln1b, Ob);
+    gemm_qkv0_kernel<<<kT / 4, 256, 0, stream>>>(Ob, Wq, Wk, Wv, bq, bk, bv, Qh, Kh, Vh);
 
     for (int l = 0; l < 4; l++) {
-        gemm_qkv_kernel<<<kT / 4, 256, 0, stream>>>(A,
-            Wq + l * kD * kD, Wk + l * kD * kD, Wv + l * kD * kD,
-            bq + l * kDG, bk + l * kDG, bv + l * kDG, Qh, Kh, Vh);
-        attn_mfma_kernel<<<dim3(4, kNH, kB), 256, 0, stream>>>(Qh, Kh, Vh, A);
-        gemmWo_fused_kernel<<<kT / 4, 256, 0, stream>>>(A, Wo + l * kD * kD, bo + l * kDG,
-            l == 0 ? x_in : X, gm1 + l * kDG, ln2w + l * kDG, ln2b + l * kDG, X, A);
-        mlp1_kernel<<<kT / 4, 256, 0, stream>>>(A, W1 + l * kE * kD, b1 + l * kE * kG, Mb);
+        attn_mfma_kernel<<<dim3(4, kNH, kB), 256, 0, stream>>>(Qh, Kh, Vh, Ob);
+        womlp1_kernel<<<kT / 4, 256, 0, stream>>>(Ob, Wo + l * kD * kD, bo + l * kDG,
+            l == 0 ? x_in : X, gm1 + l * kDG, ln2w + l * kDG, ln2b + l * kDG,
+            W1 + l * kE * kD, b1 + l * kE * kG, X, Mb);
         if (l < 3)
-            mlp2_fused_kernel<true><<<kT / 4, 256, 0, stream>>>(Mb, W2 + l * kD * kE, b2 + l * kDG,
-                X, gm2 + l * kDG, ln1w + (l + 1) * kDG, ln1b + (l + 1) * kDG, A);
+            mlp2qkv_kernel<<<kT / 4, 256, 0, stream>>>(Mb, W2 + l * kD * kE, b2 + l * kDG,
+                X, gm2 + l * kDG, ln1w + (l + 1) * kDG, ln1b + (l + 1) * kDG,
+                Wq + (l + 1) * kD * kD, Wk + (l + 1) * kD * kD, Wv + (l + 1) * kD * kD,
+                bq + (l + 1) * kDG, bk + (l + 1) * kDG, bv + (l + 1) * kDG, Qh, Kh, Vh);
         else
-            mlp2_fused_kernel<false><<<kT / 4, 256, 0, stream>>>(Mb, W2 + l * kD * kE, b2 + l * kDG,
-                X, gm2 + l * kDG, nullptr, nullptr, nullptr);
-    }
-
-    vlinT_kernel<<<kT, 256, 0, stream>>>(X, Wr, br, A);
-    scanreg_kernel<<<kB * kD / 4, 256, 0, stream>>>(A, pooled);
+            mlp2_plain_kernel<<<kT / 4, 256, 0, stream>>>(Mb, W2 + l * kD * kE, b2 + l * kDG,
+                X, gm2 + l * kDG);
+    }
+
+    vlinT_kernel<<<kT, 256, 0, stream>>>(X, Wr, br, DT);
+    scanreg_kernel<<<kB * kD / 4, 256, 0, stream>>>(DT, pooled);
     cls2_kernel<<<kNC / 4, 256, 0, stream>>>(pooled, Wc, bc, (float*)d_out);
 }
```

After: 637.4 us. +4.4%, slower.
